# Performance work log

Measured on AMD Instinct MI355X. Metric: run time of the kernel, lower is better.

## Reference

```python
import jax, jax.numpy as jnp
import numpy as np

DIM = 4096
N_HEADS = 32
N_KV_HEADS = 8
HEAD_DIM = DIM // N_HEADS  # 128
N_REP = N_HEADS // N_KV_HEADS  # 4
HIDDEN = 14336  # 4*dim -> 2/3 -> *1.3 -> round up to multiple of 256
EPS = 1e-6
BSZ, SEQLEN, CACHE_LEN = 1, 2048, 4096
ROPE_THETA = 500000.0


def setup_inputs() -> dict:
    key = jax.random.key(0)
    ks = jax.random.split(key, 16)
    s = 0.02
    x = jax.random.normal(ks[0], (BSZ, SEQLEN, DIM), jnp.float32)
    cache_k = jax.random.normal(ks[1], (BSZ, CACHE_LEN, N_KV_HEADS, HEAD_DIM), jnp.float32)
    cache_v = jax.random.normal(ks[2], (BSZ, CACHE_LEN, N_KV_HEADS, HEAD_DIM), jnp.float32)
    # causal mask over rolling cache: query i may attend to cache slot j <= (CACHE_LEN - SEQLEN) + i
    qi = jnp.arange(SEQLEN)[:, None]
    kj = jnp.arange(CACHE_LEN)[None, :]
    mask = jnp.where(kj <= (CACHE_LEN - SEQLEN) + qi, 0.0, -1e9).astype(jnp.float32)[None, None]
    # rotary freqs (cos/sin pairs) for the new seqlen positions (start of window here)
    inv = 1.0 / (ROPE_THETA ** (jnp.arange(0, HEAD_DIM, 2, dtype=jnp.float32) / HEAD_DIM))
    t = jnp.arange(SEQLEN, dtype=jnp.float32)
    ang = t[:, None] * inv[None, :]  # [S, HEAD_DIM//2]
    freqs_cis = jnp.stack([jnp.cos(ang), jnp.sin(ang)], axis=-1)  # [S, HD//2, 2]
    # params (stored as (in, out))
    wq = jax.random.normal(ks[3], (DIM, N_HEADS * HEAD_DIM), jnp.float32) * s
    wk = jax.random.normal(ks[4], (DIM, N_KV_HEADS * HEAD_DIM), jnp.float32) * s
    wv = jax.random.normal(ks[5], (DIM, N_KV_HEADS * HEAD_DIM), jnp.float32) * s
    wo = jax.random.normal(ks[6], (N_HEADS * HEAD_DIM, DIM), jnp.float32) * s
    w1 = jax.random.normal(ks[7], (DIM, HIDDEN), jnp.float32) * s
    w2 = jax.random.normal(ks[8], (HIDDEN, DIM), jnp.float32) * s
    w3 = jax.random.normal(ks[9], (DIM, HIDDEN), jnp.float32) * s
    attn_norm_w = jnp.ones((DIM,), jnp.float32)
    ffn_norm_w = jnp.ones((DIM,), jnp.float32)
    return dict(x=x, mask=mask, freqs_cis=freqs_cis, cache_k=cache_k, cache_v=cache_v,
                wq=wq, wk=wk, wv=wv, wo=wo, w1=w1, w2=w2, w3=w3,
                attn_norm_w=attn_norm_w, ffn_norm_w=ffn_norm_w)


def rmsnorm(x, w, eps=EPS):
    return x * jax.lax.rsqrt(jnp.mean(x * x, axis=-1, keepdims=True) + eps) * w


def apply_rope(xq, xk, freqs_cis):
    # xq: [B,S,Hq,D], xk: [B,S,Hkv,D]; freqs_cis: [S, D//2, 2]
    cos = freqs_cis[None, :, None, :, 0]  # [1,S,1,D//2]
    sin = freqs_cis[None, :, None, :, 1]
    def rot(t):
        tp = t.reshape(*t.shape[:-1], -1, 2)
        t0, t1 = tp[..., 0], tp[..., 1]
        o0 = t0 * cos - t1 * sin
        o1 = t0 * sin + t1 * cos
        return jnp.stack([o0, o1], axis=-1).reshape(t.shape)
    return rot(xq), rot(xk)


def reference(x, mask, freqs_cis, cache_k, cache_v, wq, wk, wv, wo, w1, w2, w3, attn_norm_w, ffn_norm_w):
    bsz, seqlen, _ = x.shape
    # --- attention norm ---
    xn = rmsnorm(x, attn_norm_w)
    # --- qkv ---
    xq = (xn @ wq).reshape(bsz, seqlen, N_HEADS, HEAD_DIM)
    xk = (xn @ wk).reshape(bsz, seqlen, N_KV_HEADS, HEAD_DIM)
    xv = (xn @ wv).reshape(bsz, seqlen, N_KV_HEADS, HEAD_DIM)
    xq, xk = apply_rope(xq, xk, freqs_cis)
    # --- rolling KV cache ---
    cache_k = jnp.concatenate([cache_k[:, seqlen:], xk], axis=1)  # [B,CL,Hkv,D]
    cache_v = jnp.concatenate([cache_v[:, seqlen:], xv], axis=1)
    keys = jnp.repeat(cache_k[:bsz], N_REP, axis=2)    # [B,CL,Hq,D]
    values = jnp.repeat(cache_v[:bsz], N_REP, axis=2)
    # --- attention ---
    scores = jnp.einsum('bqhd,bkhd->bhqk', xq, keys) / jnp.sqrt(jnp.float32(HEAD_DIM))
    scores = jax.nn.softmax(scores + mask, axis=-1)
    attn = jnp.einsum('bhqk,bkhd->bqhd', scores, values).reshape(bsz, seqlen, -1)
    h = x + attn @ wo
    # --- ffn (SwiGLU) ---
    hn = rmsnorm(h, ffn_norm_w)
    out = h + (jax.nn.silu(hn @ w1) * (hn @ w3)) @ w2
    return (out, cache_k, cache_v)
```

## Files before the change

kernel.cpp:

```cpp
#include <hip/hip_runtime.h>

typedef _Float16 h16;
typedef _Float16 h16x4 __attribute__((ext_vector_type(4)));
typedef _Float16 h16x8 __attribute__((ext_vector_type(8)));
typedef float f32x4 __attribute__((ext_vector_type(4)));
typedef float f32x16 __attribute__((ext_vector_type(16)));
typedef unsigned short u16;

__device__ __forceinline__ f32x4 mfma16(h16x8 a, h16x8 b, f32x4 c) {
  return __builtin_amdgcn_mfma_f32_16x16x32_f16(a, b, c, 0, 0, 0);
}
__device__ __forceinline__ f32x16 mfma32(h16x8 a, h16x8 b, f32x16 c) {
  return __builtin_amdgcn_mfma_f32_32x32x16_f16(a, b, c, 0, 0, 0);
}

typedef const __attribute__((address_space(1))) void* gas_p;
typedef __attribute__((address_space(3))) void* las_p;
__device__ __forceinline__ void ldscp16(const void* g, void* l) {
  __builtin_amdgcn_global_load_lds((gas_p)g, (las_p)l, 16, 0, 0);
}

__global__ __launch_bounds__(256) void rmsnorm_k(
    const float* __restrict__ x, const float* __restrict__ w, h16* __restrict__ out) {
  const int row = blockIdx.x, t = threadIdx.x;
  const float* xr = x + (size_t)row * 4096;
  float4 v[4];
  float ss = 0.f;
#pragma unroll
  for (int j = 0; j < 4; j++) {
    v[j] = *(const float4*)(xr + 4 * t + 1024 * j);
    ss += v[j].x * v[j].x + v[j].y * v[j].y + v[j].z * v[j].z + v[j].w * v[j].w;
  }
#pragma unroll
  for (int off = 1; off < 64; off <<= 1) ss += __shfl_xor(ss, off, 64);
  __shared__ float red[4];
  if ((t & 63) == 0) red[t >> 6] = ss;
  __syncthreads();
  float scale = rsqrtf((red[0] + red[1] + red[2] + red[3]) * (1.f / 4096.f) + 1e-6f);
  h16* orow = out + (size_t)row * 4096;
#pragma unroll
  for (int j = 0; j < 4; j++) {
    float4 wv = *(const float4*)(w + 4 * t + 1024 * j);
    h16x4 o;
    o[0] = (h16)(v[j].x * scale * wv.x);
    o[1] = (h16)(v[j].y * scale * wv.y);
    o[2] = (h16)(v[j].z * scale * wv.z);
    o[3] = (h16)(v[j].w * scale * wv.w);
    *(h16x4*)(orow + 4 * t + 1024 * j) = o;
  }
}

__global__ __launch_bounds__(256) void convw_k(
    const float* __restrict__ W, h16* __restrict__ out, int rowN, int ktiles) {
  __shared__ u16 timg[8192];
  const int t = threadIdx.x, b = blockIdx.x, kt = blockIdx.y;
  const float* src = W + (size_t)(kt * 64) * rowN + b * 128;
#pragma unroll
  for (int i = 0; i < 8; i++) {
    int c = t + (i << 8);
    int krow = c >> 5, nc = (c & 31) << 2;
    float4 v = *(const float4*)(src + (size_t)krow * rowN + nc);
    int kc = krow >> 3, e = krow & 7;
    float vals[4] = {v.x, v.y, v.z, v.w};
#pragma unroll
    for (int j = 0; j < 4; j++) {
      int m = nc + j;
      h16 hv = (h16)vals[j];
      timg[(m << 6) + ((kc ^ (m & 7)) << 3) + e] = __builtin_bit_cast(u16, hv);
    }
  }
  __syncthreads();
  uint4* dst = (uint4*)(out + ((size_t)(b * ktiles + kt) << 13));
  const uint4* s4 = (const uint4*)timg;
#pragma unroll
  for (int i = 0; i < 4; i++) dst[t + (i << 8)] = s4[t + (i << 8)];
}

template <int EPI>
__global__ __launch_bounds__(256, 2) void gemm_k(
    const h16* __restrict__ A, const h16* __restrict__ Wt,
    float* outF, h16* outH, const float* resid, const h16* uin,
    int K, int lda, int ldo, int no0) {
  __shared__ u16 sA[2][8192];
  __shared__ u16 sB[2][8192];
  const int tid = threadIdx.x, lane = tid & 63;
  const int wv = tid >> 6, wr = wv >> 1, wc = wv & 1;
  const int g = lane >> 4, lr = lane & 15;
  const int m0 = blockIdx.y << 7, n0 = blockIdx.x << 7;
  const int r8 = lane >> 3, ch = lane & 7;
  const int ktiles = K >> 6;

  f32x4 acc[4][4];
#pragma unroll
  for (int i = 0; i < 4; i++)
#pragma unroll
    for (int j = 0; j < 4; j++) acc[i][j] = {0.f, 0.f, 0.f, 0.f};

  const h16* gA0 = A + (size_t)(m0 + wv * 8 + r8) * lda + ((ch ^ r8) << 3);
  const h16* gB0 = Wt + ((size_t)blockIdx.x * ktiles << 13) + (wv << 9) + (lane << 3);

  auto stage = [&](int kt, int buf) {
    char* lA = (char*)sA[buf] + (wv << 10);
    char* lB = (char*)sB[buf] + (wv << 10);
    const h16* a = gA0 + kt * 64;
    const h16* b = gB0 + (size_t)kt * 8192;
#pragma unroll
    for (int i = 0; i < 4; i++) {
      ldscp16(a + (size_t)i * 32 * lda, lA + i * 4096);
      ldscp16(b + i * 2048, lB + i * 4096);
    }
  };

  stage(0, 0);
  __syncthreads();
  int cur = 0;
  for (int kt = 0; kt < ktiles; ++kt) {
    if (kt + 1 < ktiles) stage(kt + 1, cur ^ 1);
#pragma unroll
    for (int ks = 0; ks < 2; ++ks) {
      h16x8 av[4], bv[4];
#pragma unroll
      for (int f = 0; f < 4; f++) {
        int row = (wr << 6) + (f << 4) + lr;
        int cc = (ks << 2) + g;
        av[f] = *(const h16x8*)((char*)sA[cur] + row * 128 + ((cc ^ (row & 7)) << 4));
        int col = (wc << 6) + (f << 4) + lr;
        bv[f] = *(const h16x8*)((char*)sB[cur] + col * 128 + ((cc ^ (col & 7)) << 4));
      }
#pragma unroll
      for (int fi = 0; fi < 4; fi++)
#pragma unroll
        for (int fj = 0; fj < 4; fj++)
          acc[fi][fj] = mfma16(av[fi], bv[fj], acc[fi][fj]);
    }
    __syncthreads();
    cur ^= 1;
  }
#pragma unroll
  for (int fi = 0; fi < 4; fi++) {
    const int row = m0 + (wr << 6) + (fi << 4) + (g << 2);
#pragma unroll
    for (int fj = 0; fj < 4; fj++) {
      const int col = no0 + n0 + (wc << 6) + (fj << 4) + lr;
#pragma unroll
      for (int r = 0; r < 4; r++) {
        float vl = acc[fi][fj][r];
        if constexpr (EPI == 5) {
          if (col < 4096) outH[(size_t)(row + r) * 4096 + col] = (h16)vl;
          else outF[(size_t)(row + r) * 2048 + (col - 4096)] = vl;
        } else {
          size_t idx = (size_t)(row + r) * ldo + col;
          if constexpr (EPI == 0) outF[idx] = vl;
          else if constexpr (EPI == 1) outH[idx] = (h16)vl;
          else if constexpr (EPI == 2) outF[idx] = resid[idx] + vl;
          else if constexpr (EPI == 3) {
            float u = (float)uin[idx];
            outH[idx] = (h16)((u / (1.f + __expf(-u))) * vl);
          } else outF[idx] = outF[idx] + vl;
        }
      }
    }
  }
}

__global__ __launch_bounds__(256) void rope_q_k(
    const h16* __restrict__ qin, const float* __restrict__ freqs, h16* qout) {
  const int row = blockIdx.x, t = threadIdx.x;
#pragma unroll
  for (int it = 0; it < 8; ++it) {
    int pid = t + 256 * it;
    int head = pid >> 6, pp = pid & 63;
    size_t idx = (size_t)row * 4096 + head * 128 + 2 * pp;
    float x0 = (float)qin[idx], x1 = (float)qin[idx + 1];
    float cs = freqs[row * 128 + 2 * pp], sn = freqs[row * 128 + 2 * pp + 1];
    qout[idx] = (h16)(x0 * cs - x1 * sn);
    qout[idx + 1] = (h16)(x0 * sn + x1 * cs);
  }
}

__global__ __launch_bounds__(256) void cache_build_k(
    const float* __restrict__ oldK, const float* __restrict__ oldV,
    const float* __restrict__ kvraw, const float* __restrict__ freqs,
    float* __restrict__ outK, float* __restrict__ outV,
    h16* __restrict__ Kf, h16* __restrict__ Vt) {
  const int rt = blockIdx.x, kvh = blockIdx.y;
  const int r0 = rt * 64, tid = threadIdx.x;
  __shared__ u16 vtile[64][128];
#pragma unroll
  for (int it = 0; it < 16; ++it) {
    int s = tid + 256 * it;
    int rr = s >> 6, pp = s & 63;
    int r = r0 + rr;
    float k0, k1, v0, v1;
    if (r < 2048) {
      const float* kp = oldK + (size_t)(r + 2048) * 1024 + kvh * 128 + 2 * pp;
      k0 = kp[0]; k1 = kp[1];
      const float* vp = oldV + (size_t)(r + 2048) * 1024 + kvh * 128 + 2 * pp;
      v0 = vp[0]; v1 = vp[1];
    } else {
      int tpos = r - 2048;
      const float* kp = kvraw + (size_t)tpos * 2048 + kvh * 128 + 2 * pp;
      float x0 = kp[0], x1 = kp[1];
      float cs = freqs[tpos * 128 + 2 * pp], sn = freqs[tpos * 128 + 2 * pp + 1];
      k0 = x0 * cs - x1 * sn;
      k1 = x0 * sn + x1 * cs;
      const float* vp = kvraw + (size_t)tpos * 2048 + 1024 + kvh * 128 + 2 * pp;
      v0 = vp[0]; v1 = vp[1];
    }
    size_t oidx = (size_t)r * 1024 + kvh * 128 + 2 * pp;
    outK[oidx] = k0; outK[oidx + 1] = k1;
    outV[oidx] = v0; outV[oidx + 1] = v1;
    size_t kfi = (size_t)kvh * 524288 + (size_t)r * 128 + 2 * pp;
    Kf[kfi] = (h16)k0; Kf[kfi + 1] = (h16)k1;
    h16 h0 = (h16)v0, h1 = (h16)v1;
    vtile[rr][2 * pp] = __builtin_bit_cast(u16, h0);
    vtile[rr][2 * pp + 1] = __builtin_bit_cast(u16, h1);
  }
  __syncthreads();
#pragma unroll
  for (int it = 0; it < 4; ++it) {
    int c = tid + 256 * it;
    int d = c >> 3, rg = c & 7;
    u16 tmp[8];
#pragma unroll
    for (int u = 0; u < 8; u++) tmp[u] = vtile[rg * 8 + u][d];
    *(uint4*)((u16*)Vt + (size_t)kvh * 524288 + (size_t)d * 4096 + r0 + rg * 8) =
        *(uint4*)tmp;
  }
}

__global__ __launch_bounds__(256) void attn_k(
    const h16* __restrict__ Q, const h16* __restrict__ Kf,
    const h16* __restrict__ Vt, h16* __restrict__ O) {
  __shared__ u16 sK[2][8192];
  __shared__ u16 sV[2][8192];
  __shared__ u16 sP[4][2048];
  const int qt = 15 - blockIdx.x, h = blockIdx.y;
  const int q0 = qt << 7, kvh = h >> 2;
  const int tid = threadIdx.x, w = tid >> 6, lane = tid & 63;
  const int lq = lane & 31, lh = lane >> 5;
  const h16* Kb = Kf + (size_t)kvh * 524288;
  const h16* Vb = Vt + (size_t)kvh * 524288;

  h16x8 qv[8];
  {
    const h16* qp = Q + (size_t)(q0 + w * 32 + lq) * 4096 + h * 128 + (lh << 3);
#pragma unroll
    for (int c = 0; c < 8; c++) qv[c] = *(const h16x8*)(qp + c * 16);
  }
  f32x16 oa[4];
#pragma unroll
  for (int d = 0; d < 4; d++)
#pragma unroll
    for (int v = 0; v < 16; v++) oa[d][v] = 0.f;
  float m2 = -3e38f, l2 = 0.f;
  const int ntiles = 34 + 2 * qt;
  const float sc = 0.08838834764831845f;
  const int qg = q0 + w * 32 + lq;

  auto stage = [&](int buf, int j0s) {
    char* dK = (char*)sK[buf];
    char* dV = (char*)sV[buf];
#pragma unroll
    for (int i = 0; i < 4; i++) {
      int c = tid + (i << 8);
      int jl = c >> 4, kch = c & 15;
      ldscp16(Kb + (size_t)(j0s + jl) * 128 + ((kch ^ (jl & 15)) << 3), dK + c * 16);
      int dl = c >> 3, jch = c & 7;
      ldscp16(Vb + (size_t)dl * 4096 + j0s + ((jch ^ (dl & 7)) << 3), dV + c * 16);
    }
  };

  stage(0, 0);
  __syncthreads();
  int cur = 0;
  for (int jt = 0; jt < ntiles; ++jt) {
    if (jt + 1 < ntiles) stage(cur ^ 1, (jt + 1) << 6);
    const char* bK = (const char*)sK[cur];
    const char* bV = (const char*)sV[cur];
    f32x16 st[2];
#pragma unroll
    for (int jb = 0; jb < 2; jb++) {
      f32x16 s;
#pragma unroll
      for (int v = 0; v < 16; v++) s[v] = 0.f;
      const int jr = jb * 32 + lq;
#pragma unroll
      for (int kc = 0; kc < 8; kc++) {
        h16x8 ak =
            *(const h16x8*)(bK + jr * 256 + ((((kc << 1) + lh) ^ (jr & 15)) << 4));
        s = mfma32(ak, qv[kc], s);
      }
      st[jb] = s;
    }
    const int j0 = jt << 6;
    const bool domask = (jt >= ntiles - 2);
    float pm = -3e38f;
#pragma unroll
    for (int jb = 0; jb < 2; jb++)
#pragma unroll
      for (int v = 0; v < 16; v++) {
        float val = st[jb][v] * sc;
        if (domask) {
          int j = j0 + jb * 32 + (v & 3) + (((v >> 2) & 3) << 3) + (lh << 2);
          if (j > 2048 + qg) val = -1e30f;
        }
        st[jb][v] = val;
        pm = fmaxf(pm, val);
      }
    pm = fmaxf(pm, __shfl_xor(pm, 32, 64));
    if (__any(pm - m2 > 8.f)) {
      float mn = fmaxf(m2, pm);
      float al = __expf(m2 - mn);
      m2 = mn;
      l2 *= al;
#pragma unroll
      for (int d = 0; d < 4; d++) oa[d] *= al;
    }
    float rs = 0.f;
#pragma unroll
    for (int jb = 0; jb < 2; jb++)
#pragma unroll
      for (int v = 0; v < 16; v++) {
        float p = __expf(st[jb][v] - m2);
        st[jb][v] = p;
        rs += p;
      }
    rs += __shfl_xor(rs, 32, 64);
    l2 += rs;
    char* pw = (char*)sP[w];
#pragma unroll
    for (int jb = 0; jb < 2; jb++)
#pragma unroll
      for (int b = 0; b < 4; b++) {
        h16x4 ph;
#pragma unroll
        for (int i = 0; i < 4; i++) ph[i] = (h16)st[jb][(b << 2) + i];
        *(h16x4*)(pw + lq * 128 + ((((jb << 2) + b) ^ (lq & 7)) << 4) + (lh << 3)) =
            ph;
      }
    h16x8 pb[4];
#pragma unroll
    for (int kc = 0; kc < 4; kc++)
      pb[kc] = *(const h16x8*)(pw + lq * 128 + ((((kc << 1) + lh) ^ (lq & 7)) << 4));
#pragma unroll
    for (int d = 0; d < 4; d++) {
      const int dr = (d << 5) + lq;
#pragma unroll
      for (int kc = 0; kc < 4; kc++) {
        h16x8 av =
            *(const h16x8*)(bV + dr * 128 + ((((kc << 1) + lh) ^ (dr & 7)) << 4));
        oa[d] = mfma32(av, pb[kc], oa[d]);
      }
    }
    __syncthreads();
    cur ^= 1;
  }
  float rl = 1.f / l2;
  h16* Op = O + (size_t)qg * 4096 + h * 128;
#pragma unroll
  for (int d = 0; d < 4; d++)
#pragma unroll
    for (int b = 0; b < 4; b++) {
      h16x4 ov;
#pragma unroll
      for (int i = 0; i < 4; i++) ov[i] = (h16)(oa[d][(b << 2) + i] * rl);
      *(h16x4*)(Op + (d << 5) + (b << 3) + (lh << 2)) = ov;
    }
}

extern "C" void kernel_launch(void* const* d_in, const int* in_sizes, int n_in,
                              void* d_out, int out_size, void* d_ws, size_t ws_size,
                              hipStream_t stream) {
  const float* x = (const float*)d_in[0];
  const float* freqs = (const float*)d_in[2];
  const float* oldK = (const float*)d_in[3];
  const float* oldV = (const float*)d_in[4];
  const float* wq = (const float*)d_in[5];
  const float* wk = (const float*)d_in[6];
  const float* wvp = (const float*)d_in[7];
  const float* wo = (const float*)d_in[8];
  const float* w1 = (const float*)d_in[9];
  const float* w2 = (const float*)d_in[10];
  const float* w3 = (const float*)d_in[11];
  const float* anw = (const float*)d_in[12];
  const float* fnw = (const float*)d_in[13];
  float* out = (float*)d_out;
  float* outK = out + 8388608;
  float* outV = out + 12582912;

  char* ws = (char*)d_ws;
  h16* xn = (h16*)(ws + 0);
  h16* bufW = (h16*)(ws + 16777216);
  float* hbuf = (float*)(ws + 75497472);
  float* kvraw = (float*)(ws + 75497472);
  h16* kf = (h16*)(ws + 92274688);
  h16* vt = (h16*)(ws + 100663296);
  h16* ub = (h16*)(ws + 109051904);
  h16* qraw = (h16*)(ws + 109051904);
  h16* attnb = (h16*)(ws + 125829120);

  rmsnorm_k<<<2048, 256, 0, stream>>>(x, anw, xn);
  convw_k<<<dim3(32, 64), 256, 0, stream>>>(wq, bufW, 4096, 64);
  convw_k<<<dim3(8, 64), 256, 0, stream>>>(wk, bufW + ((size_t)32 * 64 << 13), 1024, 64);
  convw_k<<<dim3(8, 64), 256, 0, stream>>>(wvp, bufW + ((size_t)40 * 64 << 13), 1024, 64);
  gemm_k<5><<<dim3(48, 16), 256, 0, stream>>>(xn, bufW, kvraw, qraw, nullptr,
                                              nullptr, 4096, 4096, 0, 0);
  rope_q_k<<<2048, 256, 0, stream>>>(qraw, freqs, qraw);
  cache_build_k<<<dim3(64, 8), 256, 0, stream>>>(oldK, oldV, kvraw, freqs, outK,
                                                 outV, kf, vt);
  attn_k<<<dim3(16, 32), 256, 0, stream>>>(qraw, kf, vt, attnb);
  convw_k<<<dim3(32, 64), 256, 0, stream>>>(wo, bufW, 4096, 64);
  gemm_k<2><<<dim3(32, 16), 256, 0, stream>>>(attnb, bufW, hbuf, nullptr, x,
                                              nullptr, 4096, 4096, 4096, 0);
  rmsnorm_k<<<2048, 256, 0, stream>>>(hbuf, fnw, xn);
  convw_k<<<dim3(56, 64), 256, 0, stream>>>(w1, bufW, 14336, 64);
  gemm_k<1><<<dim3(56, 16), 256, 0, stream>>>(xn, bufW, nullptr, ub, nullptr,
                                              nullptr, 4096, 4096, 14336, 0);
  convw_k<<<dim3(56, 64), 256, 0, stream>>>(w1 + 7168, bufW, 14336, 64);
  gemm_k<1><<<dim3(56, 16), 256, 0, stream>>>(xn, bufW, nullptr, ub, nullptr,
                                              nullptr, 4096, 4096, 14336, 7168);
  convw_k<<<dim3(56, 64), 256, 0, stream>>>(w3, bufW, 14336, 64);
  gemm_k<3><<<dim3(56, 16), 256, 0, stream>>>(xn, bufW, nullptr, ub, nullptr, ub,
                                              4096, 4096, 14336, 0);
  convw_k<<<dim3(56, 64), 256, 0, stream>>>(w3 + 7168, bufW, 14336, 64);
  gemm_k<3><<<dim3(56, 16), 256, 0, stream>>>(xn, bufW, nullptr, ub, nullptr, ub,
                                              4096, 4096, 14336, 7168);
  convw_k<<<dim3(32, 112), 256, 0, stream>>>(w2, bufW, 4096, 112);
  gemm_k<2><<<dim3(32, 16), 256, 0, stream>>>(ub, bufW, out, nullptr, hbuf,
                                              nullptr, 7168, 14336, 4096, 0);
  convw_k<<<dim3(32, 112), 256, 0, stream>>>(w2 + (size_t)7168 * 4096, bufW, 4096, 112);
  gemm_k<4><<<dim3(32, 16), 256, 0, stream>>>(ub + 7168, bufW, out, nullptr,
                                              nullptr, nullptr, 7168, 14336, 4096, 0);
}
```

Baseline: 1.833 ms.

## Widen GEMM and attention blocks to 512 threads with triple-buffered async loads

The GEMM kernel now uses 8 waves per block, covering a 128x256 output tile, with a three-stage LDS ring. Global-to-LDS copies are issued two tiles ahead and gated by explicit vmcnt waits plus a single barrier per tile. The attention kernel likewise handles 256 queries per block with a three-stage shared K/V ring. It builds the P operand through cross-lane shuffles instead of an LDS round trip, and raises wave priority around MFMA sections. The aim is to hide memory latency and cut barrier and LDS traffic, at the cost of more LDS per block, possible lower occupancy, and fewer blocks for load balance.

```diff
diff --git a/kernel.cpp b/kernel.cpp
--- a/kernel.cpp
+++ b/kernel.cpp
@@ -6,6 +6,7 @@
 typedef float f32x4 __attribute__((ext_vector_type(4)));
 typedef float f32x16 __attribute__((ext_vector_type(16)));
 typedef unsigned short u16;
+typedef unsigned long long u64;
 
 __device__ __forceinline__ f32x4 mfma16(h16x8 a, h16x8 b, f32x4 c) {
   return __builtin_amdgcn_mfma_f32_16x16x32_f16(a, b, c, 0, 0, 0);
@@ -19,6 +20,8 @@
 __device__ __forceinline__ void ldscp16(const void* g, void* l) {
   __builtin_amdgcn_global_load_lds((gas_p)g, (las_p)l, 16, 0, 0);
 }
+#define VMCNT(n) asm volatile("s_waitcnt vmcnt(" #n ")" ::: "memory")
+#define SBAR() asm volatile("s_barrier" ::: "memory")
 
 __global__ __launch_bounds__(256) void rmsnorm_k(
     const float* __restrict__ x, const float* __restrict__ w, h16* __restrict__ out) {
@@ -77,17 +80,15 @@
 }
 
 template <int EPI>
-__global__ __launch_bounds__(256, 2) void gemm_k(
+__global__ __launch_bounds__(512, 2) void gemm_k(
     const h16* __restrict__ A, const h16* __restrict__ Wt,
     float* outF, h16* outH, const float* resid, const h16* uin,
     int K, int lda, int ldo, int no0) {
-  __shared__ u16 sA[2][8192];
-  __shared__ u16 sB[2][8192];
+  __shared__ u16 lds[3][24576];
   const int tid = threadIdx.x, lane = tid & 63;
-  const int wv = tid >> 6, wr = wv >> 1, wc = wv & 1;
+  const int wv = tid >> 6, wr = wv >> 2, wc = wv & 3;
   const int g = lane >> 4, lr = lane & 15;
-  const int m0 = blockIdx.y << 7, n0 = blockIdx.x << 7;
-  const int r8 = lane >> 3, ch = lane & 7;
+  const int m0 = blockIdx.y << 7, n0 = blockIdx.x << 8;
   const int ktiles = K >> 6;
 
   f32x4 acc[4][4];
@@ -96,45 +97,61 @@
 #pragma unroll
     for (int j = 0; j < 4; j++) acc[i][j] = {0.f, 0.f, 0.f, 0.f};
 
-  const h16* gA0 = A + (size_t)(m0 + wv * 8 + r8) * lda + ((ch ^ r8) << 3);
-  const h16* gB0 = Wt + ((size_t)blockIdx.x * ktiles << 13) + (wv << 9) + (lane << 3);
-
-  auto stage = [&](int kt, int buf) {
-    char* lA = (char*)sA[buf] + (wv << 10);
-    char* lB = (char*)sB[buf] + (wv << 10);
-    const h16* a = gA0 + kt * 64;
-    const h16* b = gB0 + (size_t)kt * 8192;
-#pragma unroll
-    for (int i = 0; i < 4; i++) {
-      ldscp16(a + (size_t)i * 32 * lda, lA + i * 4096);
-      ldscp16(b + i * 2048, lB + i * 4096);
-    }
+  const int rA = tid >> 3;
+  const int kcA = (tid & 7) ^ (rA & 7);
+  const h16* gA = A + (size_t)(m0 + rA) * lda + (kcA << 3);
+  const h16* gA2 = gA + (size_t)64 * lda;
+  const h16* gB0 = Wt + (((size_t)(2 * blockIdx.x) * ktiles) << 13) + tid * 8;
+  const h16* gB1 = Wt + (((size_t)(2 * blockIdx.x + 1) * ktiles) << 13) + tid * 8;
+
+  auto issueA = [&](int t) {
+    char* base = (char*)lds[t % 3];
+    ldscp16(gA + t * 64, base + tid * 16);
+    ldscp16(gA2 + t * 64, base + tid * 16 + 8192);
+    ldscp16(gB0 + ((size_t)t << 13), base + 16384 + tid * 16);
+    ldscp16(gB0 + ((size_t)t << 13) + 4096, base + 16384 + tid * 16 + 8192);
   };
-
-  stage(0, 0);
-  __syncthreads();
-  int cur = 0;
-  for (int kt = 0; kt < ktiles; ++kt) {
-    if (kt + 1 < ktiles) stage(kt + 1, cur ^ 1);
+  auto issueB = [&](int t) {
+    char* base = (char*)lds[t % 3];
+    ldscp16(gB1 + ((size_t)t << 13), base + 32768 + tid * 16);
+    ldscp16(gB1 + ((size_t)t << 13) + 4096, base + 32768 + tid * 16 + 8192);
+  };
+
+  issueA(0); issueB(0); issueA(1); issueB(1);
+  VMCNT(6);
+  SBAR();
+
+  for (int t = 0; t < ktiles; ++t) {
+    const char* bp = (const char*)lds[t % 3];
+    const bool more = (t + 2 < ktiles);
 #pragma unroll
     for (int ks = 0; ks < 2; ++ks) {
       h16x8 av[4], bv[4];
+      const int cc = (ks << 2) + g;
 #pragma unroll
       for (int f = 0; f < 4; f++) {
         int row = (wr << 6) + (f << 4) + lr;
-        int cc = (ks << 2) + g;
-        av[f] = *(const h16x8*)((char*)sA[cur] + row * 128 + ((cc ^ (row & 7)) << 4));
-        int col = (wc << 6) + (f << 4) + lr;
-        bv[f] = *(const h16x8*)((char*)sB[cur] + col * 128 + ((cc ^ (col & 7)) << 4));
-      }
+        av[f] = *(const h16x8*)(bp + row * 128 + ((cc ^ (row & 7)) << 4));
+        int nr = (wc << 6) + (f << 4) + lr;
+        bv[f] = *(const h16x8*)(bp + 16384 + nr * 128 + ((cc ^ (nr & 7)) << 4));
+      }
+      if (more) {
+        if (ks == 0) issueA(t + 2);
+        else issueB(t + 2);
+      }
+      __builtin_amdgcn_s_setprio(1);
 #pragma unroll
       for (int fi = 0; fi < 4; fi++)
 #pragma unroll
         for (int fj = 0; fj < 4; fj++)
           acc[fi][fj] = mfma16(av[fi], bv[fj], acc[fi][fj]);
-    }
-    __syncthreads();
-    cur ^= 1;
+      __builtin_amdgcn_s_setprio(0);
+    }
+    if (t + 1 < ktiles) {
+      if (more) VMCNT(6);
+      else VMCNT(0);
+      SBAR();
+    }
   }
 #pragma unroll
   for (int fi = 0; fi < 4; fi++) {
@@ -150,8 +167,7 @@
           else outF[(size_t)(row + r) * 2048 + (col - 4096)] = vl;
         } else {
           size_t idx = (size_t)(row + r) * ldo + col;
-          if constexpr (EPI == 0) outF[idx] = vl;
-          else if constexpr (EPI == 1) outH[idx] = (h16)vl;
+          if constexpr (EPI == 1) outH[idx] = (h16)vl;
           else if constexpr (EPI == 2) outF[idx] = resid[idx] + vl;
           else if constexpr (EPI == 3) {
             float u = (float)uin[idx];
@@ -229,22 +245,21 @@
   }
 }
 
-__global__ __launch_bounds__(256) void attn_k(
+__global__ __launch_bounds__(512, 2) void attn_k(
     const h16* __restrict__ Q, const h16* __restrict__ Kf,
     const h16* __restrict__ Vt, h16* __restrict__ O) {
-  __shared__ u16 sK[2][8192];
-  __shared__ u16 sV[2][8192];
-  __shared__ u16 sP[4][2048];
-  const int qt = 15 - blockIdx.x, h = blockIdx.y;
-  const int q0 = qt << 7, kvh = h >> 2;
+  __shared__ u16 skv[3][16384];
+  const int qt = blockIdx.x, h = blockIdx.y;
+  const int q0 = qt << 8, kvh = h >> 2;
   const int tid = threadIdx.x, w = tid >> 6, lane = tid & 63;
   const int lq = lane & 31, lh = lane >> 5;
   const h16* Kb = Kf + (size_t)kvh * 524288;
   const h16* Vb = Vt + (size_t)kvh * 524288;
+  const int qg = q0 + w * 32 + lq;
 
   h16x8 qv[8];
   {
-    const h16* qp = Q + (size_t)(q0 + w * 32 + lq) * 4096 + h * 128 + (lh << 3);
+    const h16* qp = Q + (size_t)qg * 4096 + h * 128 + (lh << 3);
 #pragma unroll
     for (int c = 0; c < 8; c++) qv[c] = *(const h16x8*)(qp + c * 16);
   }
@@ -254,30 +269,35 @@
 #pragma unroll
     for (int v = 0; v < 16; v++) oa[d][v] = 0.f;
   float m2 = -3e38f, l2 = 0.f;
-  const int ntiles = 34 + 2 * qt;
+  const int ntiles = 36 + 4 * qt;
   const float sc = 0.08838834764831845f;
-  const int qg = q0 + w * 32 + lq;
-
-  auto stage = [&](int buf, int j0s) {
-    char* dK = (char*)sK[buf];
-    char* dV = (char*)sV[buf];
-#pragma unroll
-    for (int i = 0; i < 4; i++) {
-      int c = tid + (i << 8);
-      int jl = c >> 4, kch = c & 15;
-      ldscp16(Kb + (size_t)(j0s + jl) * 128 + ((kch ^ (jl & 15)) << 3), dK + c * 16);
-      int dl = c >> 3, jch = c & 7;
-      ldscp16(Vb + (size_t)dl * 4096 + j0s + ((jch ^ (dl & 7)) << 3), dV + c * 16);
-    }
+
+  const int jK = tid >> 4, kchK = tid & 15;
+  const h16* gK = Kb + (size_t)jK * 128 + ((kchK ^ (jK & 15)) << 3);
+  const int dV = tid >> 3, jchV = tid & 7;
+  const h16* gV = Vb + (size_t)dV * 4096 + ((jchV ^ (dV & 7)) << 3);
+
+  auto issueK = [&](int jt) {
+    char* base = (char*)skv[jt % 3];
+    const h16* s = gK + (jt << 6) * 128;
+    ldscp16(s, base + tid * 16);
+    ldscp16(s + 32 * 128, base + tid * 16 + 8192);
   };
-
-  stage(0, 0);
-  __syncthreads();
-  int cur = 0;
+  auto issueV = [&](int jt) {
+    char* base = (char*)skv[jt % 3];
+    const h16* s = gV + (jt << 6);
+    ldscp16(s, base + 16384 + tid * 16);
+    ldscp16(s + (size_t)64 * 4096, base + 16384 + tid * 16 + 8192);
+  };
+
+  issueK(0); issueV(0); issueK(1); issueV(1);
+  VMCNT(4);
+  SBAR();
+
   for (int jt = 0; jt < ntiles; ++jt) {
-    if (jt + 1 < ntiles) stage(cur ^ 1, (jt + 1) << 6);
-    const char* bK = (const char*)sK[cur];
-    const char* bV = (const char*)sV[cur];
+    const char* bp = (const char*)skv[jt % 3];
+    const bool more = (jt + 2 < ntiles);
+    if (more) issueK(jt + 2);
     f32x16 st[2];
 #pragma unroll
     for (int jb = 0; jb < 2; jb++) {
@@ -285,16 +305,19 @@
 #pragma unroll
       for (int v = 0; v < 16; v++) s[v] = 0.f;
       const int jr = jb * 32 + lq;
+      __builtin_amdgcn_s_setprio(1);
 #pragma unroll
       for (int kc = 0; kc < 8; kc++) {
         h16x8 ak =
-            *(const h16x8*)(bK + jr * 256 + ((((kc << 1) + lh) ^ (jr & 15)) << 4));
+            *(const h16x8*)(bp + jr * 256 + ((((kc << 1) + lh) ^ (jr & 15)) << 4));
         s = mfma32(ak, qv[kc], s);
       }
+      __builtin_amdgcn_s_setprio(0);
       st[jb] = s;
     }
+    if (more) issueV(jt + 2);
     const int j0 = jt << 6;
-    const bool domask = (jt >= ntiles - 2);
+    const bool domask = (jt >= ntiles - 4);
     float pm = -3e38f;
 #pragma unroll
     for (int jb = 0; jb < 2; jb++)
@@ -328,33 +351,44 @@
       }
     rs += __shfl_xor(rs, 32, 64);
     l2 += rs;
-    char* pw = (char*)sP[w];
-#pragma unroll
-    for (int jb = 0; jb < 2; jb++)
-#pragma unroll
-      for (int b = 0; b < 4; b++) {
-        h16x4 ph;
-#pragma unroll
-        for (int i = 0; i < 4; i++) ph[i] = (h16)st[jb][(b << 2) + i];
-        *(h16x4*)(pw + lq * 128 + ((((jb << 2) + b) ^ (lq & 7)) << 4) + (lh << 3)) =
-            ph;
-      }
     h16x8 pb[4];
 #pragma unroll
-    for (int kc = 0; kc < 4; kc++)
-      pb[kc] = *(const h16x8*)(pw + lq * 128 + ((((kc << 1) + lh) ^ (lq & 7)) << 4));
+    for (int kc = 0; kc < 4; kc++) {
+      const int jb = kc >> 1, cb = (kc & 1) << 1;
+      const int cs = cb + 1 - lh, ck = cb + lh;
+      h16x4 sq, kq;
+#pragma unroll
+      for (int i = 0; i < 4; i++) {
+        sq[i] = (h16)st[jb][(cs << 2) + i];
+        kq[i] = (h16)st[jb][(ck << 2) + i];
+      }
+      u64 rv = __shfl_xor(__builtin_bit_cast(u64, sq), 32, 64);
+      h16x4 rq = __builtin_bit_cast(h16x4, rv);
+      h16x4 lo = lh ? rq : kq;
+      h16x4 hi = lh ? kq : rq;
+#pragma unroll
+      for (int i = 0; i < 4; i++) {
+        pb[kc][i] = lo[i];
+        pb[kc][i + 4] = hi[i];
+      }
+    }
+    __builtin_amdgcn_s_setprio(1);
 #pragma unroll
     for (int d = 0; d < 4; d++) {
       const int dr = (d << 5) + lq;
 #pragma unroll
       for (int kc = 0; kc < 4; kc++) {
-        h16x8 av =
-            *(const h16x8*)(bV + dr * 128 + ((((kc << 1) + lh) ^ (dr & 7)) << 4));
+        h16x8 av = *(const h16x8*)(bp + 16384 + dr * 128 +
+                                   ((((kc << 1) + lh) ^ (dr & 7)) << 4));
         oa[d] = mfma32(av, pb[kc], oa[d]);
       }
     }
-    __syncthreads();
-    cur ^= 1;
+    __builtin_amdgcn_s_setprio(0);
+    if (jt + 1 < ntiles) {
+      if (more) VMCNT(4);
+      else VMCNT(0);
+      SBAR();
+    }
   }
   float rl = 1.f / l2;
   h16* Op = O + (size_t)qg * 4096 + h * 128;
@@ -404,32 +438,32 @@
   convw_k<<<dim3(32, 64), 256, 0, stream>>>(wq, bufW, 4096, 64);
   convw_k<<<dim3(8, 64), 256, 0, stream>>>(wk, bufW + ((size_t)32 * 64 << 13), 1024, 64);
   convw_k<<<dim3(8, 64), 256, 0, stream>>>(wvp, bufW + ((size_t)40 * 64 << 13), 1024, 64);
-  gemm_k<5><<<dim3(48, 16), 256, 0, stream>>>(xn, bufW, kvraw, qraw, nullptr,
+  gemm_k<5><<<dim3(24, 16), 512, 0, stream>>>(xn, bufW, kvraw, qraw, nullptr,
                                               nullptr, 4096, 4096, 0, 0);
   rope_q_k<<<2048, 256, 0, stream>>>(qraw, freqs, qraw);
   cache_build_k<<<dim3(64, 8), 256, 0, stream>>>(oldK, oldV, kvraw, freqs, outK,
                                                  outV, kf, vt);
-  attn_k<<<dim3(16, 32), 256, 0, stream>>>(qraw, kf, vt, attnb);
+  attn_k<<<dim3(8, 32), 512, 0, stream>>>(qraw, kf, vt, attnb);
   convw_k<<<dim3(32, 64), 256, 0, stream>>>(wo, bufW, 4096, 64);
-  gemm_k<2><<<dim3(32, 16), 256, 0, stream>>>(attnb, bufW, hbuf, nullptr, x,
+  gemm_k<2><<<dim3(16, 16), 512, 0, stream>>>(attnb, bufW, hbuf, nullptr, x,
                                               nullptr, 4096, 4096, 4096, 0);
   rmsnorm_k<<<2048, 256, 0, stream>>>(hbuf, fnw, xn);
   convw_k<<<dim3(56, 64), 256, 0, stream>>>(w1, bufW, 14336, 64);
-  gemm_k<1><<<dim3(56, 16), 256, 0, stream>>>(xn, bufW, nullptr, ub, nullptr,
+  gemm_k<1><<<dim3(28, 16), 512, 0, stream>>>(xn, bufW, nullptr, ub, nullptr,
                                               nullptr, 4096, 4096, 14336, 0);
   convw_k<<<dim3(56, 64), 256, 0, stream>>>(w1 + 7168, bufW, 14336, 64);
-  gemm_k<1><<<dim3(56, 16), 256, 0, stream>>>(xn, bufW, nullptr, ub, nullptr,
+  gemm_k<1><<<dim3(28, 16), 512, 0, stream>>>(xn, bufW, nullptr, ub, nullptr,
                                               nullptr, 4096, 4096, 14336, 7168);
   convw_k<<<dim3(56, 64), 256, 0, stream>>>(w3, bufW, 14336, 64);
-  gemm_k<3><<<dim3(56, 16), 256, 0, stream>>>(xn, bufW, nullptr, ub, nullptr, ub,
+  gemm_k<3><<<dim3(28, 16), 512, 0, stream>>>(xn, bufW, nullptr, ub, nullptr, ub,
                                               4096, 4096, 14336, 0);
   convw_k<<<dim3(56, 64), 256, 0, stream>>>(w3 + 7168, bufW, 14336, 64);
-  gemm_k<3><<<dim3(56, 16), 256, 0, stream>>>(xn, bufW, nullptr, ub, nullptr, ub,
+  gemm_k<3><<<dim3(28, 16), 512, 0, stream>>>(xn, bufW, nullptr, ub, nullptr, ub,
                                               4096, 4096, 14336, 7168);
   convw_k<<<dim3(32, 112), 256, 0, stream>>>(w2, bufW, 4096, 112);
-  gemm_k<2><<<dim3(32, 16), 256, 0, stream>>>(ub, bufW, out, nullptr, hbuf,
+  gemm_k<2><<<dim3(16, 16), 512, 0, stream>>>(ub, bufW, out, nullptr, hbuf,
                                               nullptr, 7168, 14336, 4096, 0);
   convw_k<<<dim3(32, 112), 256, 0, stream>>>(w2 + (size_t)7168 * 4096, bufW, 4096, 112);
-  gemm_k<4><<<dim3(32, 16), 256, 0, stream>>>(ub + 7168, bufW, out, nullptr,
+  gemm_k<4><<<dim3(16, 16), 512, 0, stream>>>(ub + 7168, bufW, out, nullptr,
                                               nullptr, nullptr, 7168, 14336, 4096, 0);
 }
```

New measurement: 1.710 ms. 1.07x faster.
